# Kernel tuning notes

Measured on AMD Instinct MI355X. Metric: run time of the kernel, lower is better.

The kernel has to match this reference:

```python
import jax, jax.numpy as jnp
import numpy as np

N_NODES = 50000

def _sage_conv(x, src, dst, W_l, b_l, W_r):
    # mean-aggregate neighbor features: messages x[src] summed into dst
    msgs = x[src]                                   # [E, d]
    agg = jax.ops.segment_sum(msgs, dst, num_segments=N_NODES)  # [N, d]
    ones = jnp.ones((src.shape[0],), dtype=x.dtype)
    cnt = jax.ops.segment_sum(ones, dst, num_segments=N_NODES)  # [N]
    agg = agg / jnp.maximum(cnt, 1.0)[:, None]
    return agg @ W_l + b_l + x @ W_r


def setup_inputs() -> dict:
    key = jax.random.key(0)
    ks = jax.random.split(key, 8)
    d_in, hid, out = 64, 128, 64
    x = jax.random.normal(ks[0], (N_NODES, d_in), dtype=jnp.float32)
    edge_index = jax.random.randint(ks[1], (2, 1600000), 0, N_NODES, dtype=jnp.int64)
    def w(k, a, b):
        return jax.random.normal(k, (a, b), dtype=jnp.float32) / np.sqrt(a)
    return {
        "x": x,
        "edge_index": edge_index,
        "W_l1": w(ks[2], d_in, hid), "b_l1": jnp.zeros((hid,), jnp.float32),
        "W_r1": w(ks[3], d_in, hid),
        "W_l2": w(ks[4], hid, hid), "b_l2": jnp.zeros((hid,), jnp.float32),
        "W_r2": w(ks[5], hid, hid),
        "W_out": w(ks[6], hid, out), "b_out": jnp.zeros((out,), jnp.float32),
    }


def reference(x, edge_index, W_l1, b_l1, W_r1, W_l2, b_l2, W_r2, W_out, b_out):
    src, dst = edge_index[0], edge_index[1]
    h = jax.nn.relu(_sage_conv(x, src, dst, W_l1, b_l1, W_r1))
    h = jax.nn.relu(_sage_conv(h, src, dst, W_l2, b_l2, W_r2))
    return h @ W_out + b_out
```

## Files before the change

### kernel.cpp

```cpp
#include <hip/hip_runtime.h>


typedef unsigned short ushort_t;
typedef unsigned int uint_t;
typedef unsigned char uchar_t;
typedef __attribute__((ext_vector_type(8))) short short8;
typedef __attribute__((ext_vector_type(8))) ushort_t ushort8;
typedef __attribute__((ext_vector_type(4))) float f32x4;

#define BKT_SHIFT 7
#define BKT_NODES 128
#define BKT_CAP   5120
#define EPB       4096
#define QSCALE    32.0f
#define QINV      0.03125f
#define XQSCALE   16.0f

__device__ inline ushort_t bf16_rne(float v) {
    uint_t u = __float_as_uint(v);
    u += 0x7fffu + ((u >> 16) & 1u);
    return (ushort_t)(u >> 16);
}
__device__ inline float bf16_to_f(ushort_t h) {
    return __uint_as_float((uint_t)h << 16);
}


struct WPack {
    const float* srcp[5];
    ushort_t* dstp[5];
    int K[5], N[5], beg[5], end[5];
};

__global__ __launch_bounds__(1024)
void k_work(const int* __restrict__ src, const int* __restrict__ dst,
            uint_t* __restrict__ pairs, int* __restrict__ bcnt, int E, int nbk,
            int bbl, const float* __restrict__ x, ushort_t* __restrict__ xh,
            uchar_t* __restrict__ xq, int NS, WPack wp, int total) {
    int tid = threadIdx.x;
    if (blockIdx.x >= bbl) {
        int t = (blockIdx.x - bbl) * 1024 + tid;
        if (t < NS) {
            float v = x[t];
            xh[t] = bf16_rne(v);
            int qv = (int)(v * XQSCALE + 128.5f);
            qv = qv < 0 ? 0 : (qv > 255 ? 255 : qv);
            xq[t] = (uchar_t)qv;
            return;
        }
        t -= NS;
        if (t >= total) return;
#pragma unroll
        for (int m = 0; m < 5; ++m) {
            if (t >= wp.beg[m] && t < wp.end[m]) {
                int i = t - wp.beg[m];
                int K = wp.K[m], N = wp.N[m];
                int k = i / N, nn = i % N;
                int NT = N >> 4;
                int kt = k >> 5, bq = (k >> 3) & 3, j = k & 7;
                int nt = nn >> 4, lane = (bq << 4) | (nn & 15);
                int base = (((kt * NT + nt) << 6) + lane) * 8 + j;
                int halfsz = (K >> 5) * NT * 512;
                float v = wp.srcp[m][i];
                ushort_t h = bf16_rne(v);
                wp.dstp[m][base] = h;
                wp.dstp[m][halfsz + base] = bf16_rne(v - bf16_to_f(h));
            }
        }
        return;
    }

    __shared__ int h[4][512];
    int sub = tid & 3;
    for (int i = tid; i < 4 * 512; i += 1024) ((int*)h)[i] = 0;
    __syncthreads();

    int e = blockIdx.x * EPB + tid * 4;
    bool full = (e + 4 <= E);
    int4 d4 = {0, 0, 0, 0}, s4 = {0, 0, 0, 0};
    if (full) {
        d4 = *(const int4*)(dst + e);
        s4 = *(const int4*)(src + e);
        atomicAdd(&h[sub][d4.x >> BKT_SHIFT], 1);
        atomicAdd(&h[sub][d4.y >> BKT_SHIFT], 1);
        atomicAdd(&h[sub][d4.z >> BKT_SHIFT], 1);
        atomicAdd(&h[sub][d4.w >> BKT_SHIFT], 1);
    } else {
        for (int t = e; t < E && t < e + 4; ++t)
            atomicAdd(&h[sub][dst[t] >> BKT_SHIFT], 1);
    }
    __syncthreads();
    for (int i = tid; i < nbk; i += 1024) {
        int c0 = h[0][i], c1 = h[1][i], c2 = h[2][i], c3 = h[3][i];
        int c = c0 + c1 + c2 + c3;
        int bs = c ? atomicAdd(&bcnt[i], c) : 0;
        h[0][i] = bs; h[1][i] = bs + c0; h[2][i] = bs + c0 + c1;
        h[3][i] = bs + c0 + c1 + c2;
    }
    __syncthreads();
    if (full) {
        int dd[4] = {d4.x, d4.y, d4.z, d4.w};
        int ss[4] = {s4.x, s4.y, s4.z, s4.w};
#pragma unroll
        for (int t = 0; t < 4; ++t) {
            int b = dd[t] >> BKT_SHIFT;
            int r = atomicAdd(&h[sub][b], 1);
            pairs[(size_t)b * BKT_CAP + r] =
                (uint_t)(ss[t] & 0xFFFF) | ((uint_t)(dd[t] & (BKT_NODES - 1)) << 16);
        }
    } else {
        for (int t = e; t < E && t < e + 4; ++t) {
            int d = dst[t];
            int b = d >> BKT_SHIFT;
            int r = atomicAdd(&h[sub][b], 1);
            pairs[(size_t)b * BKT_CAP + r] =
                (uint_t)(src[t] & 0xFFFF) | ((uint_t)(d & (BKT_NODES - 1)) << 16);
        }
    }
}


__global__ __launch_bounds__(1024) void k_csr(const uint_t* __restrict__ pairs,
                                              const int* __restrict__ bcnt,
                                              int* __restrict__ off,
                                              ushort_t* __restrict__ col, int n) {
    __shared__ int hist[BKT_NODES];
    __shared__ int s[BKT_NODES];
    __shared__ int cur[BKT_NODES];
    __shared__ int bofs_s;
    int b = blockIdx.x, tid = threadIdx.x;
    if (tid < 64) {
        int p = 0;
        for (int i = tid; i < b; i += 64) p += bcnt[i];
#pragma unroll
        for (int m = 1; m < 64; m <<= 1) p += __shfl_xor(p, m);
        if (tid == 0) bofs_s = p;
    }
    if (tid < BKT_NODES) hist[tid] = 0;
    __syncthreads();
    int bofs = bofs_s;
    int cnt = bcnt[b];
    const uint_t* p = pairs + (size_t)b * BKT_CAP;
    for (int i = tid; i < cnt; i += 1024) atomicAdd(&hist[(p[i] >> 16) & 127], 1);
    __syncthreads();
    int v = (tid < BKT_NODES) ? hist[tid] : 0;
    if (tid < BKT_NODES) s[tid] = v;
    __syncthreads();
    for (int ofs = 1; ofs < BKT_NODES; ofs <<= 1) {
        int t = (tid >= ofs && tid < BKT_NODES) ? s[tid - ofs] : 0;
        __syncthreads();
        if (tid < BKT_NODES) s[tid] += t;
        __syncthreads();
    }
    if (tid < BKT_NODES) {
        int excl = bofs + s[tid] - v;
        int node = b * BKT_NODES + tid;
        if (node <= n) off[node] = excl;
        cur[tid] = excl;
    }
    __syncthreads();
    for (int i = tid; i < cnt; i += 1024) {
        uint_t pk = p[i];
        int pos = atomicAdd(&cur[(pk >> 16) & 127], 1);
        col[pos] = (ushort_t)(pk & 0xFFFF);
    }
}

__device__ inline f32x4 mfma3(f32x4 acc, short8 ah, short8 al, short8 bh, short8 bl) {
    acc = __builtin_amdgcn_mfma_f32_16x16x32_bf16(ah, bh, acc, 0, 0, 0);
    acc = __builtin_amdgcn_mfma_f32_16x16x32_bf16(al, bh, acc, 0, 0, 0);
    acc = __builtin_amdgcn_mfma_f32_16x16x32_bf16(ah, bl, acc, 0, 0, 0);
    return acc;
}


__global__ __launch_bounds__(256, 4)
void k_layer1(const uchar_t* __restrict__ xq, const ushort_t* __restrict__ xh,
              const int* __restrict__ off, const ushort_t* __restrict__ col,
              const ushort_t* __restrict__ Wlp, const ushort_t* __restrict__ Wrp,
              const float* __restrict__ bias, uchar_t* __restrict__ Oq, int n) {
    __shared__ ushort_t SB[9216];
    ushort_t* Ahs = SB;
    ushort_t* Als = SB + 64 * 72;
    int tid = threadIdx.x, waveid = tid >> 6, lane = tid & 63;
    int base = blockIdx.x * 64;
    int grp = lane >> 2, li = lane & 3;
    int nl = waveid * 16 + grp;
    int node = base + nl;
    int nd = node < n ? node : n - 1;
    int s0 = off[nd], s1 = off[nd + 1], last = s1 - 1;
    uint_t ae[4] = {0, 0, 0, 0}, ao[4] = {0, 0, 0, 0};
    const uchar_t* fb = xq + li * 16;
    int e = s0;
    for (; e + 8 <= s1; e += 8) {
        int c[8];
#pragma unroll
        for (int j = 0; j < 8; ++j) c[j] = col[e + j];
        uint4 q[8];
#pragma unroll
        for (int j = 0; j < 8; ++j) q[j] = *(const uint4*)(fb + (size_t)c[j] * 64);
#pragma unroll
        for (int j = 0; j < 8; ++j) {
            const uint_t* u = (const uint_t*)&q[j];
#pragma unroll
            for (int k = 0; k < 4; ++k) {
                ae[k] += u[k] & 0x00FF00FFu;
                ao[k] += (u[k] >> 8) & 0x00FF00FFu;
            }
        }
    }
    if (e < s1) {
        int c[8];
        uint_t msk[8];
#pragma unroll
        for (int j = 0; j < 8; ++j) {
            int idx = e + j;
            msk[j] = (idx < s1) ? 0xFFFFFFFFu : 0u;
            c[j] = col[min(idx, last)];
        }
        uint4 q[8];
#pragma unroll
        for (int j = 0; j < 8; ++j) q[j] = *(const uint4*)(fb + (size_t)c[j] * 64);
#pragma unroll
        for (int j = 0; j < 8; ++j) {
            const uint_t* u = (const uint_t*)&q[j];
#pragma unroll
            for (int k = 0; k < 4; ++k) {
                uint_t v = u[k] & msk[j];
                ae[k] += v & 0x00FF00FFu;
                ao[k] += (v >> 8) & 0x00FF00FFu;
            }
        }
    }
    {
        int deg = s1 - s0;
        float inv = 1.f / (XQSCALE * fmaxf((float)deg, 1.f));
        float c8 = deg > 0 ? 8.f : 0.f;
        ushort_t vh[16], vl[16];
#pragma unroll
        for (int k = 0; k < 4; ++k) {
            uint_t f[4] = {ae[k] & 0xFFFFu, ao[k] & 0xFFFFu,
                           ae[k] >> 16, ao[k] >> 16};
#pragma unroll
            for (int b = 0; b < 4; ++b) {
                float v = (float)f[b] * inv - c8;
                ushort_t h = bf16_rne(v);
                vh[k * 4 + b] = h;
                vl[k * 4 + b] = bf16_rne(v - bf16_to_f(h));
            }
        }
        *(ushort8*)&Ahs[nl * 72 + li * 16] = *(ushort8*)&vh[0];
        *(ushort8*)&Ahs[nl * 72 + li * 16 + 8] = *(ushort8*)&vh[8];
        *(ushort8*)&Als[nl * 72 + li * 16] = *(ushort8*)&vl[0];
        *(ushort8*)&Als[nl * 72 + li * 16 + 8] = *(ushort8*)&vl[8];
    }
    __syncthreads();

    int rowt = waveid;
    int colq = lane & 15, quad = lane >> 4;
    int arow = rowt * 16 + colq;
    short8 fah[2], fal[2], fxh[2];
#pragma unroll
    for (int kt = 0; kt < 2; ++kt) {
        fah[kt] = *(const short8*)&Ahs[arow * 72 + kt * 32 + quad * 8];
        fal[kt] = *(const short8*)&Als[arow * 72 + kt * 32 + quad * 8];
    }
    int grow = base + arow; if (grow >= n) grow = n - 1;
#pragma unroll
    for (int kt = 0; kt < 2; ++kt)
        fxh[kt] = *(const short8*)(xh + (size_t)grow * 64 + kt * 32 + quad * 8);
    __syncthreads();

    ushort_t* OT = SB;
#pragma unroll
    for (int nt = 0; nt < 8; ++nt) {
        float bv = bias[nt * 16 + colq];
        f32x4 acc = (f32x4){bv, bv, bv, bv};
#pragma unroll
        for (int kt = 0; kt < 2; ++kt) {
            const ushort_t* pL = Wlp + ((size_t)((kt * 8 + nt) << 6) + lane) * 8;
            acc = mfma3(acc, fah[kt], fal[kt],
                        *(const short8*)pL, *(const short8*)(pL + 8192));
            const ushort_t* pR = Wrp + ((size_t)((kt * 8 + nt) << 6) + lane) * 8;
            short8 bh = *(const short8*)pR;
            short8 bl = *(const short8*)(pR + 8192);
            acc = __builtin_amdgcn_mfma_f32_16x16x32_bf16(fxh[kt], bh, acc, 0, 0, 0);
            acc = __builtin_amdgcn_mfma_f32_16x16x32_bf16(fxh[kt], bl, acc, 0, 0, 0);
        }
        int lrb = rowt * 16 + quad * 4;
        int cix = nt * 16 + colq;
#pragma unroll
        for (int r = 0; r < 4; ++r)
            OT[(lrb + r) * 136 + cix] = bf16_rne(fmaxf(acc[r], 0.f));
    }
    __syncthreads();

#pragma unroll
    for (int it = 0; it < 4; ++it) {
        int idx = it * 256 + tid;
        int lr = idx >> 4;
        int cc = (idx & 15) * 8;
        int row = base + lr;
        if (row < n) {
            ushort8 v8 = *(ushort8*)&OT[lr * 136 + cc];
            uchar_t qb[8];
#pragma unroll
            for (int j = 0; j < 8; ++j) {
                float v = bf16_to_f((ushort_t)v8[j]);
                int qv = (int)(v * QSCALE + 0.5f);
                qb[j] = (uchar_t)(qv > 255 ? 255 : qv);
            }
            *(uint2*)(Oq + (size_t)row * 128 + cc) = *(uint2*)qb;
        }
    }
}


__global__ __launch_bounds__(256, 4)
void k_layer2(const uchar_t* __restrict__ h1q, const int* __restrict__ off,
              const ushort_t* __restrict__ col,
              const ushort_t* __restrict__ Wlp, const ushort_t* __restrict__ Wrp,
              const float* __restrict__ b2, const ushort_t* __restrict__ Wop,
              const float* __restrict__ bo, float* __restrict__ out, int n) {
    __shared__ ushort_t SB[8704];
    ushort_t* Ah = SB;
    ushort_t* Al = SB + 32 * 136;
    int tid = threadIdx.x, waveid = tid >> 6, lane = tid & 63;
    int base = blockIdx.x * 32;
    int grp = lane >> 3, li = lane & 7;
    int nl = waveid * 8 + grp;
    int node = base + nl;
    int nd = node < n ? node : n - 1;
    int s0 = off[nd], s1 = off[nd + 1], last = s1 - 1;
    uint_t ae[4] = {0, 0, 0, 0}, ao[4] = {0, 0, 0, 0};
    const uchar_t* fb = h1q + li * 16;
    int e = s0;
    for (; e + 16 <= s1; e += 16) {
        int c[16];
#pragma unroll
        for (int j = 0; j < 16; ++j) c[j] = col[e + j];
        uint4 q[16];
#pragma unroll
        for (int j = 0; j < 16; ++j)
            q[j] = *(const uint4*)(fb + (size_t)c[j] * 128);
#pragma unroll
        for (int j = 0; j < 16; ++j) {
            const uint_t* u = (const uint_t*)&q[j];
#pragma unroll
            for (int k = 0; k < 4; ++k) {
                ae[k] += u[k] & 0x00FF00FFu;
                ao[k] += (u[k] >> 8) & 0x00FF00FFu;
            }
        }
    }
    if (e + 8 <= s1) {
        int c[8];
#pragma unroll
        for (int j = 0; j < 8; ++j) c[j] = col[e + j];
        uint4 q[8];
#pragma unroll
        for (int j = 0; j < 8; ++j) q[j] = *(const uint4*)(fb + (size_t)c[j] * 128);
#pragma unroll
        for (int j = 0; j < 8; ++j) {
            const uint_t* u = (const uint_t*)&q[j];
#pragma unroll
            for (int k = 0; k < 4; ++k) {
                ae[k] += u[k] & 0x00FF00FFu;
                ao[k] += (u[k] >> 8) & 0x00FF00FFu;
            }
        }
        e += 8;
    }
    if (e < s1) {
        int c[8];
        uint_t msk[8];
#pragma unroll
        for (int j = 0; j < 8; ++j) {
            int idx = e + j;
            msk[j] = (idx < s1) ? 0xFFFFFFFFu : 0u;
            c[j] = col[min(idx, last)];
        }
        uint4 q[8];
#pragma unroll
        for (int j = 0; j < 8; ++j) q[j] = *(const uint4*)(fb + (size_t)c[j] * 128);
#pragma unroll
        for (int j = 0; j < 8; ++j) {
            const uint_t* u = (const uint_t*)&q[j];
#pragma unroll
            for (int k = 0; k < 4; ++k) {
                uint_t v = u[k] & msk[j];
                ae[k] += v & 0x00FF00FFu;
                ao[k] += (v >> 8) & 0x00FF00FFu;
            }
        }
    }
    {
        float inv = QINV / fmaxf((float)(s1 - s0), 1.f);
        ushort_t vh[16], vl[16];
#pragma unroll
        for (int k = 0; k < 4; ++k) {
            uint_t f[4] = {ae[k] & 0xFFFFu, ao[k] & 0xFFFFu,
                           ae[k] >> 16, ao[k] >> 16};
#pragma unroll
            for (int b = 0; b < 4; ++b) {
                float v = (float)f[b] * inv;
                ushort_t h = bf16_rne(v);
                vh[k * 4 + b] = h;
                vl[k * 4 + b] = bf16_rne(v - bf16_to_f(h));
            }
        }
        *(ushort8*)&Ah[nl * 136 + li * 16] = *(ushort8*)&vh[0];
        *(ushort8*)&Ah[nl * 136 + li * 16 + 8] = *(ushort8*)&vh[8];
        *(ushort8*)&Al[nl * 136 + li * 16] = *(ushort8*)&vl[0];
        *(ushort8*)&Al[nl * 136 + li * 16 + 8] = *(ushort8*)&vl[8];
    }
    __syncthreads();

    int rowt = waveid >> 1, c0w = waveid & 1;
    int colx = lane & 15, quad = lane >> 4;
    int arow = rowt * 16 + colx;
    int grow = base + arow; if (grow >= n) grow = n - 1;
    short8 gah[4], gal[4], sh[4];
#pragma unroll
    for (int kt = 0; kt < 4; ++kt) {
        gah[kt] = *(const short8*)&Ah[arow * 136 + kt * 32 + quad * 8];
        gal[kt] = *(const short8*)&Al[arow * 136 + kt * 32 + quad * 8];
        uint2 qv2 = *(const uint2*)(h1q + (size_t)grow * 128 + kt * 32 + quad * 8);
        const uchar_t* qb = (const uchar_t*)&qv2;
        ushort_t sb[8];
#pragma unroll
        for (int j = 0; j < 8; ++j)
            sb[j] = bf16_rne((float)qb[j] * QINV);
        sh[kt] = *(short8*)sb;
    }
    __syncthreads();

    f32x4 accd[4];
#pragma unroll
    for (int t = 0; t < 4; ++t) {
        int nt = t * 2 + c0w;
        float bv = b2[nt * 16 + colx];
        f32x4 acc = (f32x4){bv, bv, bv, bv};
#pragma unroll
        for (int kt = 0; kt < 4; ++kt) {
            const ushort_t* pL = Wlp + ((size_t)((kt * 8 + nt) << 6) + lane) * 8;
            acc = mfma3(acc, gah[kt], gal[kt],
                        *(const short8*)pL, *(const short8*)(pL + 16384));
            const ushort_t* pR = Wrp + ((size_t)((kt * 8 + nt) << 6) + lane) * 8;
            short8 bh = *(const short8*)pR;
            short8 bl = *(const short8*)(pR + 16384);
            acc = __builtin_amdgcn_mfma_f32_16x16x32_bf16(sh[kt], bh, acc, 0, 0, 0);
            acc = __builtin_amdgcn_mfma_f32_16x16x32_bf16(sh[kt], bl, acc, 0, 0, 0);
        }
        accd[t] = acc;
    }
#pragma unroll
    for (int t = 0; t < 4; ++t) {
        int nt = t * 2 + c0w;
#pragma unroll
        for (int r = 0; r < 4; ++r) {
            int row = rowt * 16 + quad * 4 + r;
            float v = fmaxf(accd[t][r], 0.f);
            ushort_t h = bf16_rne(v);
            Ah[row * 136 + nt * 16 + colx] = h;
            Al[row * 136 + nt * 16 + colx] = bf16_rne(v - bf16_to_f(h));
        }
    }
    __syncthreads();

    int rowt2 = waveid >> 1;
    int arow2 = rowt2 * 16 + colx;
    short8 hh[4], hl[4];
#pragma unroll
    for (int kt = 0; kt < 4; ++kt) {
        hh[kt] = *(const short8*)&Ah[arow2 * 136 + kt * 32 + quad * 8];
        hl[kt] = *(const short8*)&Al[arow2 * 136 + kt * 32 + quad * 8];
    }
    __syncthreads();

    float* OF = (float*)SB;
#pragma unroll
    for (int t2 = 0; t2 < 2; ++t2) {
        int nt2 = t2 * 2 + (waveid & 1);
        float bv = bo[nt2 * 16 + colx];
        f32x4 acc2 = (f32x4){bv, bv, bv, bv};
#pragma unroll
        for (int kt = 0; kt < 4; ++kt) {
            const ushort_t* p = Wop + ((size_t)((kt * 4 + nt2) << 6) + lane) * 8;
            acc2 = mfma3(acc2, hh[kt], hl[kt],
                         *(const short8*)p, *(const short8*)(p + 8192));
        }
#pragma unroll
        for (int r = 0; r < 4; ++r)
            OF[(rowt2 * 16 + quad * 4 + r) * 68 + nt2 * 16 + colx] = acc2[r];
    }
    __syncthreads();

#pragma unroll
    for (int it = 0; it < 2; ++it) {
        int idx = it * 256 + tid;
        int lr = idx >> 4;
        int cc = (idx & 15) * 4;
        int row = base + lr;
        if (row < n) {
            float4 v = *(float4*)&OF[lr * 68 + cc];
            *(float4*)(out + (size_t)row * 64 + cc) = v;
        }
    }
}


static inline size_t align256(size_t x) { return (x + 255) & ~(size_t)255; }

extern "C" void kernel_launch(void* const* d_in, const int* in_sizes, int n_in,
                              void* d_out, int out_size, void* d_ws, size_t ws_size,
                              hipStream_t stream) {
    const float* x   = (const float*)d_in[0];
    const int*   ei  = (const int*)d_in[1];
    const float* Wl1 = (const float*)d_in[2];
    const float* bl1 = (const float*)d_in[3];
    const float* Wr1 = (const float*)d_in[4];
    const float* Wl2 = (const float*)d_in[5];
    const float* bl2 = (const float*)d_in[6];
    const float* Wr2 = (const float*)d_in[7];
    const float* Wo  = (const float*)d_in[8];
    const float* bo  = (const float*)d_in[9];

    const int N = in_sizes[0] / 64;
    const int E = in_sizes[1] / 2;
    const int* src = ei;
    const int* dst = ei + E;
    const int nbk = (N + BKT_NODES - 1) >> BKT_SHIFT;

    char* ws = (char*)d_ws;
    int* off = (int*)ws;            ws += align256((size_t)(N + 1) * 4);
    int* bcnt = (int*)ws;           ws += align256((size_t)nbk * 4);
    uint_t* pairs = (uint_t*)ws;    ws += align256((size_t)nbk * BKT_CAP * 4);
    ushort_t* col = (ushort_t*)ws;  ws += align256((size_t)E * 2);
    ushort_t* xh  = (ushort_t*)ws;  ws += align256((size_t)N * 64 * 2);
    uchar_t*  xq  = (uchar_t*)ws;   ws += align256((size_t)N * 64);
    uchar_t*  h1q = (uchar_t*)ws;   ws += align256((size_t)N * 128);
    ushort_t* Wl1p = (ushort_t*)ws; ws += align256((size_t)2 * 64 * 128 * 2);
    ushort_t* Wr1p = (ushort_t*)ws; ws += align256((size_t)2 * 64 * 128 * 2);
    ushort_t* Wl2p = (ushort_t*)ws; ws += align256((size_t)2 * 128 * 128 * 2);
    ushort_t* Wr2p = (ushort_t*)ws; ws += align256((size_t)2 * 128 * 128 * 2);
    ushort_t* Wop  = (ushort_t*)ws; ws += align256((size_t)2 * 128 * 64 * 2);

    WPack wp;
    wp.srcp[0] = Wl1; wp.dstp[0] = Wl1p; wp.K[0] = 64;  wp.N[0] = 128;
    wp.srcp[1] = Wr1; wp.dstp[1] = Wr1p; wp.K[1] = 64;  wp.N[1] = 128;
    wp.srcp[2] = Wl2; wp.dstp[2] = Wl2p; wp.K[2] = 128; wp.N[2] = 128;
    wp.srcp[3] = Wr2; wp.dstp[3] = Wr2p; wp.K[3] = 128; wp.N[3] = 128;
    wp.srcp[4] = Wo;  wp.dstp[4] = Wop;  wp.K[4] = 128; wp.N[4] = 64;
    int acc_el = 0;
    for (int m = 0; m < 5; ++m) {
        wp.beg[m] = acc_el; acc_el += wp.K[m] * wp.N[m]; wp.end[m] = acc_el;
    }
    int NS = N * 64;

    hipMemsetAsync(bcnt, 0, (size_t)nbk * 4, stream);
    int bbl = (E + EPB - 1) / EPB;
    int pbl = (NS + acc_el + 1023) / 1024;
    k_work<<<bbl + pbl, 1024, 0, stream>>>(src, dst, pairs, bcnt, E, nbk, bbl,
                                           x, xh, xq, NS, wp, acc_el);

    k_csr<<<nbk, 1024, 0, stream>>>(pairs, bcnt, off, col, N);

    k_layer1<<<(N + 63) / 64, 256, 0, stream>>>(xq, xh, off, col, Wl1p,
                                                Wr1p, bl1, h1q, N);

    k_layer2<<<(N + 31) / 32, 256, 0, stream>>>(h1q, off, col, Wl2p, Wr2p,
                                                bl2, Wop, bo,
                                                (float*)d_out, N);
}
```

Baseline: 193.8 us.

## Sort nodes by degree so layer blocks process similar-degree nodes together

Adds a single-block counting-sort kernel that orders nodes by in-degree, highest first, and both layer kernels now map block rows through this permutation. The intent is to reduce load imbalance between lanes and waves in the neighbor-gather loops, since nodes with similar degree then share a wave. The cost is an extra serial single-block launch over all nodes and scattered, non-contiguous output writes. Tail blocks now write duplicate rows for the clamped last node, which is harmless because the values are identical.

```diff
diff --git a/kernel.cpp b/kernel.cpp
--- a/kernel.cpp
+++ b/kernel.cpp
@@ -166,6 +166,35 @@
     }
 }
 
+
+__global__ __launch_bounds__(1024)
+void k_perm(const int* __restrict__ off, int* __restrict__ perm, int n) {
+    __shared__ int hist[256];
+    __shared__ int pfx[256];
+    int tid = threadIdx.x;
+    if (tid < 256) hist[tid] = 0;
+    __syncthreads();
+    for (int i = tid; i < n; i += 1024) {
+        int d = off[i + 1] - off[i];
+        d = d > 255 ? 255 : d;
+        atomicAdd(&hist[d], 1);
+    }
+    __syncthreads();
+    if (tid == 0) {
+        int acc = 0;
+        for (int b = 255; b >= 0; --b) { pfx[b] = acc; acc += hist[b]; }
+    }
+    __syncthreads();
+    if (tid < 256) hist[tid] = pfx[tid];
+    __syncthreads();
+    for (int i = tid; i < n; i += 1024) {
+        int d = off[i + 1] - off[i];
+        d = d > 255 ? 255 : d;
+        int p = atomicAdd(&hist[d], 1);
+        perm[p] = i;
+    }
+}
+
 __device__ inline f32x4 mfma3(f32x4 acc, short8 ah, short8 al, short8 bh, short8 bl) {
     acc = __builtin_amdgcn_mfma_f32_16x16x32_bf16(ah, bh, acc, 0, 0, 0);
     acc = __builtin_amdgcn_mfma_f32_16x16x32_bf16(al, bh, acc, 0, 0, 0);
@@ -177,17 +206,20 @@
 __global__ __launch_bounds__(256, 4)
 void k_layer1(const uchar_t* __restrict__ xq, const ushort_t* __restrict__ xh,
               const int* __restrict__ off, const ushort_t* __restrict__ col,
+              const int* __restrict__ perm,
               const ushort_t* __restrict__ Wlp, const ushort_t* __restrict__ Wrp,
               const float* __restrict__ bias, uchar_t* __restrict__ Oq, int n) {
     __shared__ ushort_t SB[9216];
+    __shared__ int pm[64];
     ushort_t* Ahs = SB;
     ushort_t* Als = SB + 64 * 72;
     int tid = threadIdx.x, waveid = tid >> 6, lane = tid & 63;
     int base = blockIdx.x * 64;
+    if (tid < 64) pm[tid] = perm[min(base + tid, n - 1)];
+    __syncthreads();
     int grp = lane >> 2, li = lane & 3;
     int nl = waveid * 16 + grp;
-    int node = base + nl;
-    int nd = node < n ? node : n - 1;
+    int nd = pm[nl];
     int s0 = off[nd], s1 = off[nd + 1], last = s1 - 1;
     uint_t ae[4] = {0, 0, 0, 0}, ao[4] = {0, 0, 0, 0};
     const uchar_t* fb = xq + li * 16;
@@ -265,7 +297,7 @@
         fah[kt] = *(const short8*)&Ahs[arow * 72 + kt * 32 + quad * 8];
         fal[kt] = *(const short8*)&Als[arow * 72 + kt * 32 + quad * 8];
     }
-    int grow = base + arow; if (grow >= n) grow = n - 1;
+    int grow = pm[arow];
 #pragma unroll
     for (int kt = 0; kt < 2; ++kt)
         fxh[kt] = *(const short8*)(xh + (size_t)grow * 64 + kt * 32 + quad * 8);
@@ -300,37 +332,37 @@
         int idx = it * 256 + tid;
         int lr = idx >> 4;
         int cc = (idx & 15) * 8;
-        int row = base + lr;
-        if (row < n) {
-            ushort8 v8 = *(ushort8*)&OT[lr * 136 + cc];
-            uchar_t qb[8];
-#pragma unroll
-            for (int j = 0; j < 8; ++j) {
-                float v = bf16_to_f((ushort_t)v8[j]);
-                int qv = (int)(v * QSCALE + 0.5f);
-                qb[j] = (uchar_t)(qv > 255 ? 255 : qv);
-            }
-            *(uint2*)(Oq + (size_t)row * 128 + cc) = *(uint2*)qb;
-        }
+        int row = pm[lr];
+        ushort8 v8 = *(ushort8*)&OT[lr * 136 + cc];
+        uchar_t qb[8];
+#pragma unroll
+        for (int j = 0; j < 8; ++j) {
+            float v = bf16_to_f((ushort_t)v8[j]);
+            int qv = (int)(v * QSCALE + 0.5f);
+            qb[j] = (uchar_t)(qv > 255 ? 255 : qv);
+        }
+        *(uint2*)(Oq + (size_t)row * 128 + cc) = *(uint2*)qb;
     }
 }
 
 
 __global__ __launch_bounds__(256, 4)
 void k_layer2(const uchar_t* __restrict__ h1q, const int* __restrict__ off,
-              const ushort_t* __restrict__ col,
+              const ushort_t* __restrict__ col, const int* __restrict__ perm,
               const ushort_t* __restrict__ Wlp, const ushort_t* __restrict__ Wrp,
               const float* __restrict__ b2, const ushort_t* __restrict__ Wop,
               const float* __restrict__ bo, float* __restrict__ out, int n) {
     __shared__ ushort_t SB[8704];
+    __shared__ int pm[32];
     ushort_t* Ah = SB;
     ushort_t* Al = SB + 32 * 136;
     int tid = threadIdx.x, waveid = tid >> 6, lane = tid & 63;
     int base = blockIdx.x * 32;
+    if (tid < 32) pm[tid] = perm[min(base + tid, n - 1)];
+    __syncthreads();
     int grp = lane >> 3, li = lane & 7;
     int nl = waveid * 8 + grp;
-    int node = base + nl;
-    int nd = node < n ? node : n - 1;
+    int nd = pm[nl];
     int s0 = off[nd], s1 = off[nd + 1], last = s1 - 1;
     uint_t ae[4] = {0, 0, 0, 0}, ao[4] = {0, 0, 0, 0};
     const uchar_t* fb = h1q + li * 16;
@@ -419,7 +451,7 @@
     int rowt = waveid >> 1, c0w = waveid & 1;
     int colx = lane & 15, quad = lane >> 4;
     int arow = rowt * 16 + colx;
-    int grow = base + arow; if (grow >= n) grow = n - 1;
+    int grow = pm[arow];
     short8 gah[4], gal[4], sh[4];
 #pragma unroll
     for (int kt = 0; kt < 4; ++kt) {
@@ -501,11 +533,9 @@
         int idx = it * 256 + tid;
         int lr = idx >> 4;
         int cc = (idx & 15) * 4;
-        int row = base + lr;
-        if (row < n) {
-            float4 v = *(float4*)&OF[lr * 68 + cc];
-            *(float4*)(out + (size_t)row * 64 + cc) = v;
-        }
+        int row = pm[lr];
+        float4 v = *(float4*)&OF[lr * 68 + cc];
+        *(float4*)(out + (size_t)row * 64 + cc) = v;
     }
 }
 
@@ -534,6 +564,7 @@
 
     char* ws = (char*)d_ws;
     int* off = (int*)ws;            ws += align256((size_t)(N + 1) * 4);
+    int* perm = (int*)ws;           ws += align256((size_t)N * 4);
     int* bcnt = (int*)ws;           ws += align256((size_t)nbk * 4);
     uint_t* pairs = (uint_t*)ws;    ws += align256((size_t)nbk * BKT_CAP * 4);
     ushort_t* col = (ushort_t*)ws;  ws += align256((size_t)E * 2);
@@ -566,10 +597,12 @@
 
     k_csr<<<nbk, 1024, 0, stream>>>(pairs, bcnt, off, col, N);
 
-    k_layer1<<<(N + 63) / 64, 256, 0, stream>>>(xq, xh, off, col, Wl1p,
+    k_perm<<<1, 1024, 0, stream>>>(off, perm, N);
+
+    k_layer1<<<(N + 63) / 64, 256, 0, stream>>>(xq, xh, off, col, perm, Wl1p,
                                                 Wr1p, bl1, h1q, N);
 
-    k_layer2<<<(N + 31) / 32, 256, 0, stream>>>(h1q, off, col, Wl2p, Wr2p,
-                                                bl2, Wop, bo,
+    k_layer2<<<(N + 31) / 32, 256, 0, stream>>>(h1q, off, col, perm, Wl2p,
+                                                Wr2p, bl2, Wop, bo,
                                                 (float*)d_out, N);
 }
```

Result: slower. 229.3 us (+18.3%).

## Sort nodes by degree within each block and vectorize input conversion

Applied to the files above, without the earlier changes.

Each layer kernel now runs a wave-level bitonic sort on node degree at block start and maps rows through that permutation. Nodes with similar degree then share a wave, which evens out the gather loop lengths across lanes and cuts divergence in the neighbor aggregation. The x-to-bf16/uint8 conversion in the setup kernel also switches to float4 loads with packed stores, using a quarter as many threads. The sort adds a barrier and one extra degree read per block, and it scatters output row writes within each block.

```diff
diff --git a/kernel.cpp b/kernel.cpp
--- a/kernel.cpp
+++ b/kernel.cpp
@@ -36,19 +36,29 @@
 void k_work(const int* __restrict__ src, const int* __restrict__ dst,
             uint_t* __restrict__ pairs, int* __restrict__ bcnt, int E, int nbk,
             int bbl, const float* __restrict__ x, ushort_t* __restrict__ xh,
-            uchar_t* __restrict__ xq, int NS, WPack wp, int total) {
+            uchar_t* __restrict__ xq, int NS4, WPack wp, int total) {
     int tid = threadIdx.x;
     if (blockIdx.x >= bbl) {
         int t = (blockIdx.x - bbl) * 1024 + tid;
-        if (t < NS) {
-            float v = x[t];
-            xh[t] = bf16_rne(v);
-            int qv = (int)(v * XQSCALE + 128.5f);
-            qv = qv < 0 ? 0 : (qv > 255 ? 255 : qv);
-            xq[t] = (uchar_t)qv;
+        if (t < NS4) {
+            float4 v4 = *(const float4*)(x + (size_t)t * 4);
+            float vv[4] = {v4.x, v4.y, v4.z, v4.w};
+            ushort_t hs[4];
+            uint_t qp = 0;
+#pragma unroll
+            for (int j = 0; j < 4; ++j) {
+                hs[j] = bf16_rne(vv[j]);
+                int qv = (int)(vv[j] * XQSCALE + 128.5f);
+                qv = qv < 0 ? 0 : (qv > 255 ? 255 : qv);
+                qp |= (uint_t)qv << (8 * j);
+            }
+            uint2 hv = {(uint_t)hs[0] | ((uint_t)hs[1] << 16),
+                        (uint_t)hs[2] | ((uint_t)hs[3] << 16)};
+            *(uint2*)(xh + (size_t)t * 4) = hv;
+            *(uint_t*)(xq + (size_t)t * 4) = qp;
             return;
         }
-        t -= NS;
+        t -= NS4;
         if (t >= total) return;
 #pragma unroll
         for (int m = 0; m < 5; ++m) {
@@ -166,6 +176,29 @@
     }
 }
 
+
+template <int NK>
+__device__ inline void degsort(const int* __restrict__ off, int base, int n,
+                               int lane, int* __restrict__ pm) {
+    int deg = 0;
+    int node = base + lane;
+    if (lane < NK && node < n) deg = off[node + 1] - off[node];
+    int key = (deg << 6) | lane;
+#pragma unroll
+    for (int k = 2; k <= NK; k <<= 1) {
+#pragma unroll
+        for (int j = k >> 1; j > 0; j >>= 1) {
+            int o = __shfl_xor(key, j);
+            int mn = key < o ? key : o;
+            int mx = key < o ? o : key;
+            bool asc = (lane & k) == 0;
+            bool lower = (lane & j) == 0;
+            key = (lower == asc) ? mn : mx;
+        }
+    }
+    if (lane < NK) pm[NK - 1 - lane] = key & 63;
+}
+
 __device__ inline f32x4 mfma3(f32x4 acc, short8 ah, short8 al, short8 bh, short8 bl) {
     acc = __builtin_amdgcn_mfma_f32_16x16x32_bf16(ah, bh, acc, 0, 0, 0);
     acc = __builtin_amdgcn_mfma_f32_16x16x32_bf16(al, bh, acc, 0, 0, 0);
@@ -180,13 +213,16 @@
               const ushort_t* __restrict__ Wlp, const ushort_t* __restrict__ Wrp,
               const float* __restrict__ bias, uchar_t* __restrict__ Oq, int n) {
     __shared__ ushort_t SB[9216];
+    __shared__ int pm[64];
     ushort_t* Ahs = SB;
     ushort_t* Als = SB + 64 * 72;
     int tid = threadIdx.x, waveid = tid >> 6, lane = tid & 63;
     int base = blockIdx.x * 64;
+    if (waveid == 0) degsort<64>(off, base, n, lane, pm);
+    __syncthreads();
     int grp = lane >> 2, li = lane & 3;
     int nl = waveid * 16 + grp;
-    int node = base + nl;
+    int node = base + pm[nl];
     int nd = node < n ? node : n - 1;
     int s0 = off[nd], s1 = off[nd + 1], last = s1 - 1;
     uint_t ae[4] = {0, 0, 0, 0}, ao[4] = {0, 0, 0, 0};
@@ -265,7 +301,7 @@
         fah[kt] = *(const short8*)&Ahs[arow * 72 + kt * 32 + quad * 8];
         fal[kt] = *(const short8*)&Als[arow * 72 + kt * 32 + quad * 8];
     }
-    int grow = base + arow; if (grow >= n) grow = n - 1;
+    int grow = base + pm[arow]; if (grow >= n) grow = n - 1;
 #pragma unroll
     for (int kt = 0; kt < 2; ++kt)
         fxh[kt] = *(const short8*)(xh + (size_t)grow * 64 + kt * 32 + quad * 8);
@@ -300,7 +336,7 @@
         int idx = it * 256 + tid;
         int lr = idx >> 4;
         int cc = (idx & 15) * 8;
-        int row = base + lr;
+        int row = base + pm[lr];
         if (row < n) {
             ushort8 v8 = *(ushort8*)&OT[lr * 136 + cc];
             uchar_t qb[8];
@@ -323,13 +359,16 @@
               const float* __restrict__ b2, const ushort_t* __restrict__ Wop,
               const float* __restrict__ bo, float* __restrict__ out, int n) {
     __shared__ ushort_t SB[8704];
+    __shared__ int pm[32];
     ushort_t* Ah = SB;
     ushort_t* Al = SB + 32 * 136;
     int tid = threadIdx.x, waveid = tid >> 6, lane = tid & 63;
     int base = blockIdx.x * 32;
+    if (waveid == 0) degsort<32>(off, base, n, lane, pm);
+    __syncthreads();
     int grp = lane >> 3, li = lane & 7;
     int nl = waveid * 8 + grp;
-    int node = base + nl;
+    int node = base + pm[nl];
     int nd = node < n ? node : n - 1;
     int s0 = off[nd], s1 = off[nd + 1], last = s1 - 1;
     uint_t ae[4] = {0, 0, 0, 0}, ao[4] = {0, 0, 0, 0};
@@ -419,7 +458,7 @@
     int rowt = waveid >> 1, c0w = waveid & 1;
     int colx = lane & 15, quad = lane >> 4;
     int arow = rowt * 16 + colx;
-    int grow = base + arow; if (grow >= n) grow = n - 1;
+    int grow = base + pm[arow]; if (grow >= n) grow = n - 1;
     short8 gah[4], gal[4], sh[4];
 #pragma unroll
     for (int kt = 0; kt < 4; ++kt) {
@@ -501,7 +540,7 @@
         int idx = it * 256 + tid;
         int lr = idx >> 4;
         int cc = (idx & 15) * 4;
-        int row = base + lr;
+        int row = base + pm[lr];
         if (row < n) {
             float4 v = *(float4*)&OF[lr * 68 + cc];
             *(float4*)(out + (size_t)row * 64 + cc) = v;
@@ -556,13 +595,13 @@
     for (int m = 0; m < 5; ++m) {
         wp.beg[m] = acc_el; acc_el += wp.K[m] * wp.N[m]; wp.end[m] = acc_el;
     }
-    int NS = N * 64;
+    int NS4 = (N * 64) / 4;
 
     hipMemsetAsync(bcnt, 0, (size_t)nbk * 4, stream);
     int bbl = (E + EPB - 1) / EPB;
-    int pbl = (NS + acc_el + 1023) / 1024;
+    int pbl = (NS4 + acc_el + 1023) / 1024;
     k_work<<<bbl + pbl, 1024, 0, stream>>>(src, dst, pairs, bcnt, E, nbk, bbl,
-                                           x, xh, xq, NS, wp, acc_el);
+                                           x, xh, xq, NS4, wp, acc_el);
 
     k_csr<<<nbk, 1024, 0, stream>>>(pairs, bcnt, off, col, N);
 
```

After: 188.6 us, median of 2. 2.7% less time.
